# Kernel optimization log

Hardware: AMD Instinct MI355X
Metric: run time of the kernel (lower is better)

## Reference

```python
import jax, jax.numpy as jnp
import numpy as np

N = 50000
E = 800000
D_IN = 128
H = 256
L = 3


def setup_inputs() -> dict:
    key = jax.random.key(0)
    ks = jax.random.split(key, 12)
    x = jax.random.normal(ks[0], (N, D_IN), dtype=jnp.float32)
    edge_index = jax.random.randint(ks[1], (2, E), 0, N, dtype=jnp.int32)
    edge_attr = jax.random.uniform(ks[2], (E, 4), dtype=jnp.float32)
    s_enc = 1.0 / np.sqrt(D_IN)
    s_h = 1.0 / np.sqrt(H)
    W_enc = jax.random.uniform(ks[3], (D_IN, H), minval=-s_enc, maxval=s_enc)
    b_enc = jax.random.uniform(ks[4], (H,), minval=-s_enc, maxval=s_enc)
    W_g = jax.random.uniform(ks[5], (L, H, H), minval=-s_h, maxval=s_h)
    b_g = jax.random.uniform(ks[6], (L, H), minval=-s_h, maxval=s_h)
    W_out = jax.random.uniform(ks[7], (H, H), minval=-s_h, maxval=s_h)
    b_out = jax.random.uniform(ks[8], (H,), minval=-s_h, maxval=s_h)
    return {"x": x, "edge_index": edge_index, "edge_attr": edge_attr,
            "W_enc": W_enc, "b_enc": b_enc, "W_g": W_g, "b_g": b_g,
            "W_out": W_out, "b_out": b_out}


def _gcn_norm(edge_index, n):
    # PyG GCNConv: add self-loops, symmetric normalization D^-1/2 (A+I) D^-1/2
    loops = jnp.arange(n, dtype=edge_index.dtype)
    src = jnp.concatenate([edge_index[0], loops])  # [E+N]
    dst = jnp.concatenate([edge_index[1], loops])  # [E+N]
    deg = jax.ops.segment_sum(jnp.ones_like(dst, dtype=jnp.float32), dst, num_segments=n)
    dinv = jnp.where(deg > 0, jax.lax.rsqrt(deg), 0.0)
    norm = dinv[src] * dinv[dst]  # [E+N]
    return src, dst, norm


def _gcn_conv(h, W, b, src, dst, norm, n):
    m = h @ W                                  # [N,H] transform first
    agg = jax.ops.segment_sum(m[src] * norm[:, None], dst, num_segments=n)
    return agg + b


def reference(x, edge_index, edge_attr, W_enc, b_enc, W_g, b_g, W_out, b_out):
    n = x.shape[0]
    src, dst, norm = _gcn_norm(edge_index, n)
    h = jax.nn.relu(x @ W_enc + b_enc)
    for i in range(W_g.shape[0]):
        h = jax.nn.relu(_gcn_conv(h, W_g[i], b_g[i], src, dst, norm, n))
        # dropout is identity in eval mode
    return h @ W_out + b_out
```

## Files before the change

kernel.cpp:

```cpp
#include <hip/hip_runtime.h>
#include <math.h>

#define N_NODES 50000
#define N_EDGES 800000
#define D_IN    128
#define H_DIM   256
#define L_LAYERS 3
#define SCAN_BLOCKS ((N_NODES + 255) / 256)
#define FUSED_BLOCKS (N_NODES / 16)

typedef _Float16 f16x8 __attribute__((ext_vector_type(8)));
typedef _Float16 f16x4 __attribute__((ext_vector_type(4)));
typedef float    f32x4 __attribute__((ext_vector_type(4)));


__global__ __launch_bounds__(256) void hist_kernel(const int* __restrict__ dst,
                                                   int* __restrict__ counts,
                                                   int* __restrict__ rank, int e_cnt) {
    int e = blockIdx.x * 256 + threadIdx.x;
    if (e < e_cnt) rank[e] = atomicAdd(&counts[dst[e]], 1);
}

__global__ __launch_bounds__(256) void scanA_kernel(const int* __restrict__ counts,
                                                    int* __restrict__ blocksum,
                                                    float* __restrict__ dinv, int n) {
    __shared__ int s[256];
    int t = threadIdx.x;
    int i = blockIdx.x * 256 + t;
    int v = (i < n) ? counts[i] : 0;
    if (i < n) dinv[i] = rsqrtf((float)(v + 1));
    s[t] = v;
    __syncthreads();
#pragma unroll
    for (int d = 128; d > 0; d >>= 1) {
        if (t < d) s[t] += s[t + d];
        __syncthreads();
    }
    if (t == 0) blocksum[blockIdx.x] = s[0];
}

__global__ __launch_bounds__(256) void scanB_kernel(int* __restrict__ blocksum,
                                                    int* __restrict__ offsets,
                                                    int nblocks, int n, int total) {
    __shared__ int s[256];
    int t = threadIdx.x;
    int v = (t < nblocks) ? blocksum[t] : 0;
    s[t] = v;
    __syncthreads();
#pragma unroll
    for (int d = 1; d < 256; d <<= 1) {
        int x = (t >= d) ? s[t - d] : 0;
        __syncthreads();
        s[t] += x;
        __syncthreads();
    }
    if (t < nblocks) blocksum[t] = s[t] - v;
    if (t == 0) offsets[n] = total;
}

__global__ __launch_bounds__(256) void scanC_kernel(const int* __restrict__ counts,
                                                    const int* __restrict__ blocksum,
                                                    int* __restrict__ offsets, int n) {
    __shared__ int s[256];
    int t = threadIdx.x;
    int i = blockIdx.x * 256 + t;
    int v = (i < n) ? counts[i] : 0;
    s[t] = v;
    __syncthreads();
#pragma unroll
    for (int d = 1; d < 256; d <<= 1) {
        int x = (t >= d) ? s[t - d] : 0;
        __syncthreads();
        s[t] += x;
        __syncthreads();
    }
    if (i < n) offsets[i] = blocksum[blockIdx.x] + s[t] - v;
}

__global__ __launch_bounds__(256) void fill_kernel(const int* __restrict__ src,
                                                   const int* __restrict__ dst,
                                                   const int* __restrict__ offsets,
                                                   const int* __restrict__ rank,
                                                   const float* __restrict__ dinv,
                                                   int2* __restrict__ csr, int e_cnt) {
    int e = blockIdx.x * 256 + threadIdx.x;
    if (e < e_cnt) {
        int d = dst[e];
        int pos = offsets[d] + rank[e];
        int s = src[e];
        csr[pos] = make_int2(s, __float_as_int(dinv[s]));
    }
}


__global__ __launch_bounds__(256) void fused_layer(const _Float16* __restrict__ h_in,
                                                   const int* __restrict__ offsets,
                                                   const int2* __restrict__ csr,
                                                   const float* __restrict__ dinv,
                                                   const _Float16* __restrict__ WhL,
                                                   const _Float16* __restrict__ WlL,
                                                   const float* __restrict__ bias,
                                                   _Float16* __restrict__ h_out) {
    __shared__ _Float16 Alds[16][264];
    int wave = threadIdx.x >> 6;
    int lane = threadIdx.x & 63;
    int nb = blockIdx.x * 16;
    int c = lane * 4;

    for (int i = 0; i < 4; ++i) {
        int v = nb + 4 * wave + i;
        float dv = dinv[v];
        f16x4 self = *(const f16x4*)(h_in + (size_t)v * H_DIM + c);
        float ax = dv * (float)self[0];
        float ay = dv * (float)self[1];
        float az = dv * (float)self[2];
        float aw = dv * (float)self[3];

        int e  = offsets[v];
        int e1 = offsets[v + 1];

        for (; e + 15 < e1; e += 16) {
            int2 rec[16]; f16x4 r_[16];
#pragma unroll
            for (int j = 0; j < 16; ++j) rec[j] = csr[e + j];
#pragma unroll
            for (int j = 0; j < 16; ++j) r_[j] = *(const f16x4*)(h_in + (size_t)rec[j].x * H_DIM + c);
#pragma unroll
            for (int j = 0; j < 16; ++j) {
                float w = __int_as_float(rec[j].y);
                ax += w * (float)r_[j][0];
                ay += w * (float)r_[j][1];
                az += w * (float)r_[j][2];
                aw += w * (float)r_[j][3];
            }
        }
        if (e + 7 < e1) {
            int2 rec[8]; f16x4 r_[8];
#pragma unroll
            for (int j = 0; j < 8; ++j) rec[j] = csr[e + j];
#pragma unroll
            for (int j = 0; j < 8; ++j) r_[j] = *(const f16x4*)(h_in + (size_t)rec[j].x * H_DIM + c);
#pragma unroll
            for (int j = 0; j < 8; ++j) {
                float w = __int_as_float(rec[j].y);
                ax += w * (float)r_[j][0];
                ay += w * (float)r_[j][1];
                az += w * (float)r_[j][2];
                aw += w * (float)r_[j][3];
            }
            e += 8;
        }
        if (e + 3 < e1) {
            int2 rec[4]; f16x4 r_[4];
#pragma unroll
            for (int j = 0; j < 4; ++j) rec[j] = csr[e + j];
#pragma unroll
            for (int j = 0; j < 4; ++j) r_[j] = *(const f16x4*)(h_in + (size_t)rec[j].x * H_DIM + c);
#pragma unroll
            for (int j = 0; j < 4; ++j) {
                float w = __int_as_float(rec[j].y);
                ax += w * (float)r_[j][0];
                ay += w * (float)r_[j][1];
                az += w * (float)r_[j][2];
                aw += w * (float)r_[j][3];
            }
            e += 4;
        }
        if (e + 1 < e1) {
            int2 r0 = csr[e], r1 = csr[e + 1];
            f16x4 a = *(const f16x4*)(h_in + (size_t)r0.x * H_DIM + c);
            f16x4 b = *(const f16x4*)(h_in + (size_t)r1.x * H_DIM + c);
            float w0 = __int_as_float(r0.y), w1 = __int_as_float(r1.y);
            ax += w0 * (float)a[0] + w1 * (float)b[0];
            ay += w0 * (float)a[1] + w1 * (float)b[1];
            az += w0 * (float)a[2] + w1 * (float)b[2];
            aw += w0 * (float)a[3] + w1 * (float)b[3];
            e += 2;
        }
        if (e < e1) {
            int2 r0 = csr[e];
            f16x4 a = *(const f16x4*)(h_in + (size_t)r0.x * H_DIM + c);
            float w0 = __int_as_float(r0.y);
            ax += w0 * (float)a[0]; ay += w0 * (float)a[1];
            az += w0 * (float)a[2]; aw += w0 * (float)a[3];
        }
        f16x4 o;
        o[0] = (_Float16)(ax * dv);
        o[1] = (_Float16)(ay * dv);
        o[2] = (_Float16)(az * dv);
        o[3] = (_Float16)(aw * dv);
        *(f16x4*)&Alds[4 * wave + i][c] = o;
    }
    __syncthreads();

    int mrow = lane & 15;
    int g    = lane >> 4;
    const _Float16* Wh = WhL + (size_t)wave * 2048 + (size_t)lane * 8;
    const _Float16* Wl = WlL + (size_t)wave * 2048 + (size_t)lane * 8;

    f32x4 acc2[4];
#pragma unroll
    for (int cc = 0; cc < 4; ++cc) acc2[cc] = (f32x4)(0.0f);

#pragma unroll
    for (int kc = 0; kc < 8; ++kc) {
        f16x8 a = *(const f16x8*)&Alds[mrow][kc * 32 + g * 8];
#pragma unroll
        for (int cc = 0; cc < 4; ++cc) {
            f16x8 bh = *(const f16x8*)(Wh + kc * 8192 + cc * 512);
            f16x8 bl = *(const f16x8*)(Wl + kc * 8192 + cc * 512);
            acc2[cc] = __builtin_amdgcn_mfma_f32_16x16x32_f16(a, bh, acc2[cc], 0, 0, 0);
            acc2[cc] = __builtin_amdgcn_mfma_f32_16x16x32_f16(a, bl, acc2[cc], 0, 0, 0);
        }
    }

    int colq = lane & 15;
    int rowq = g * 4;
#pragma unroll
    for (int cc = 0; cc < 4; ++cc) {
        int col = wave * 64 + cc * 16 + colq;
        float b = bias[col];
#pragma unroll
        for (int r = 0; r < 4; ++r) {
            float vv = acc2[cc][r] + b;
            vv = fmaxf(vv, 0.f);
            h_out[(size_t)(nb + rowq + r) * H_DIM + col] = (_Float16)vv;
        }
    }
}


#define WCONV_TOTAL 294912

__global__ __launch_bounds__(256) void wconv_kernel(const float* __restrict__ W_enc,
                                                    const float* __restrict__ W_g,
                                                    const float* __restrict__ W_out,
                                                    _Float16* __restrict__ whi,
                                                    _Float16* __restrict__ wlo) {
    int gid = blockIdx.x * 256 + threadIdx.x;
    if (gid >= WCONV_TOTAL) return;
    const float* src; int base, e;
    if (gid < 32768)       { src = W_enc; base = 0;      e = gid; }
    else if (gid < 229376) { src = W_g;   base = 32768;  e = gid - 32768; }
    else                   { src = W_out; base = 229376; e = gid - 229376; }
    int k = e >> 8;
    int n = e & 255;
    float x = src[e];
    _Float16 hb = (_Float16)x;
    _Float16 lb = (_Float16)(x - (float)hb);
    int dst = base + (k >> 5) * 8192 + (n >> 4) * 512 + ((k & 31) >> 3) * 128
            + (n & 15) * 8 + (k & 7);
    whi[dst] = hb;
    wlo[dst] = lb;
}


template <int KC, int AMODE, int OUT16>
__global__ __launch_bounds__(256, 4) void mfma_gemm(const float* __restrict__ Af,
                                                    const _Float16* __restrict__ A16,
                                                    const _Float16* __restrict__ WhG,
                                                    const _Float16* __restrict__ WlG,
                                                    const float* __restrict__ bias,
                                                    float* __restrict__ Cf,
                                                    _Float16* __restrict__ Ch,
                                                    int n, int relu) {
    constexpr int K   = KC * 32;
    constexpr int PKC = (KC >= 8) ? 4 : KC;
    constexpr int NPH = KC / PKC;
    __shared__ _Float16 Wlds[PKC * 2 * 2048];

    int t = threadIdx.x;
    int w = t >> 6;
    int lane = t & 63;
    int q  = blockIdx.x >> 8;
    int rt = blockIdx.x & 255;
    if (rt * 256 >= n) return;
    int colbase = q * 64;
    int mrow = lane & 15;
    int koct = (lane >> 4) * 8;
    int rbase = rt * 256 + w * 64;

    int rows[4];
#pragma unroll
    for (int mt = 0; mt < 4; ++mt) {
        int r = rbase + mt * 16 + mrow;
        rows[mt] = (r < n) ? r : (n - 1);
    }

    f32x4 acc[4][4];
#pragma unroll
    for (int mt = 0; mt < 4; ++mt)
#pragma unroll
        for (int c = 0; c < 4; ++c)
            acc[mt][c] = (f32x4)(0.0f);

    f16x8 a16p[2][4];
    float4 af0[4], af1[4];
    if (AMODE == 1) {
#pragma unroll
        for (int mt = 0; mt < 4; ++mt) {
            a16p[0][mt] = *(const f16x8*)(A16 + (size_t)rows[mt] * K + koct);
            a16p[1][mt] = *(const f16x8*)(A16 + (size_t)rows[mt] * K + 32 + koct);
        }
    } else {
#pragma unroll
        for (int mt = 0; mt < 4; ++mt) {
            const float* p = Af + (size_t)rows[mt] * K + koct;
            af0[mt] = *(const float4*)p;
            af1[mt] = *(const float4*)(p + 4);
        }
    }

#pragma unroll
    for (int ph = 0; ph < NPH; ++ph) {
        if (ph) __syncthreads();
#pragma unroll
        for (int pk = 0; pk < PKC; ++pk) {
            int kc = ph * PKC + pk;
            __builtin_amdgcn_global_load_lds(
                (const __attribute__((address_space(1))) unsigned int*)(WhG + (size_t)kc * 8192 + q * 2048 + t * 8),
                (__attribute__((address_space(3))) unsigned int*)(&Wlds[(pk * 2 + 0) * 2048 + t * 8]), 16, 0, 0);
            __builtin_amdgcn_global_load_lds(
                (const __attribute__((address_space(1))) unsigned int*)(WlG + (size_t)kc * 8192 + q * 2048 + t * 8),
                (__attribute__((address_space(3))) unsigned int*)(&Wlds[(pk * 2 + 1) * 2048 + t * 8]), 16, 0, 0);
        }
        __syncthreads();

#pragma unroll
        for (int pk = 0; pk < PKC; ++pk) {
            int kc = ph * PKC + pk;
            f16x8 ah[4], al[4];
            if (AMODE == 0) {
#pragma unroll
                for (int mt = 0; mt < 4; ++mt) {
                    float4 c0 = af0[mt], c1 = af1[mt];
                    if (kc + 1 < KC) {
                        const float* p = Af + (size_t)rows[mt] * K + (kc + 1) * 32 + koct;
                        af0[mt] = *(const float4*)p;
                        af1[mt] = *(const float4*)(p + 4);
                    }
                    float xs[8] = {c0.x, c0.y, c0.z, c0.w, c1.x, c1.y, c1.z, c1.w};
                    f16x8 H, L;
#pragma unroll
                    for (int j = 0; j < 8; ++j) {
                        _Float16 hb = (_Float16)xs[j];
                        H[j] = hb;
                        L[j] = (_Float16)(xs[j] - (float)hb);
                    }
                    ah[mt] = H;
                    al[mt] = L;
                }
            }

#pragma unroll
            for (int c = 0; c < 4; ++c) {
                f16x8 bh = *(const f16x8*)&Wlds[(pk * 2 + 0) * 2048 + c * 512 + lane * 8];
                f16x8 bl = *(const f16x8*)&Wlds[(pk * 2 + 1) * 2048 + c * 512 + lane * 8];
#pragma unroll
                for (int mt = 0; mt < 4; ++mt) {
                    if (AMODE == 1) {
                        f16x8 a = a16p[kc & 1][mt];
                        acc[mt][c] = __builtin_amdgcn_mfma_f32_16x16x32_f16(a, bh, acc[mt][c], 0, 0, 0);
                        acc[mt][c] = __builtin_amdgcn_mfma_f32_16x16x32_f16(a, bl, acc[mt][c], 0, 0, 0);
                    } else {
                        acc[mt][c] = __builtin_amdgcn_mfma_f32_16x16x32_f16(ah[mt], bh, acc[mt][c], 0, 0, 0);
                        acc[mt][c] = __builtin_amdgcn_mfma_f32_16x16x32_f16(ah[mt], bl, acc[mt][c], 0, 0, 0);
                        acc[mt][c] = __builtin_amdgcn_mfma_f32_16x16x32_f16(al[mt], bh, acc[mt][c], 0, 0, 0);
                    }
                }
            }

            if (AMODE == 1 && kc + 2 < KC) {
#pragma unroll
                for (int mt = 0; mt < 4; ++mt)
                    a16p[kc & 1][mt] = *(const f16x8*)(A16 + (size_t)rows[mt] * K + (kc + 2) * 32 + koct);
            }
        }
    }

    int colq = lane & 15;
    int rowq = (lane >> 4) * 4;
#pragma unroll
    for (int c = 0; c < 4; ++c) {
        int col = colbase + c * 16 + colq;
        float b = bias[col];
#pragma unroll
        for (int mt = 0; mt < 4; ++mt) {
            int rb = rbase + mt * 16 + rowq;
#pragma unroll
            for (int r = 0; r < 4; ++r) {
                int row = rb + r;
                if (row < n) {
                    float v = acc[mt][c][r] + b;
                    if (relu) v = fmaxf(v, 0.f);
                    if (OUT16) Ch[(size_t)row * H_DIM + col] = (_Float16)v;
                    else       Cf[(size_t)row * H_DIM + col] = v;
                }
            }
        }
    }
}


extern "C" void kernel_launch(void* const* d_in, const int* in_sizes, int n_in,
                              void* d_out, int out_size, void* d_ws, size_t ws_size,
                              hipStream_t stream) {
    const float* x     = (const float*)d_in[0];
    const int*   ei    = (const int*)d_in[1];
    const float* W_enc = (const float*)d_in[3];
    const float* b_enc = (const float*)d_in[4];
    const float* W_g   = (const float*)d_in[5];
    const float* b_g   = (const float*)d_in[6];
    const float* W_out = (const float*)d_in[7];
    const float* b_out = (const float*)d_in[8];
    float* out = (float*)d_out;

    char* ws = (char*)d_ws;
    size_t off = 0;
    auto alloc = [&](size_t bytes) -> void* {
        void* p = ws + off;
        off = (off + bytes + 255) & ~(size_t)255;
        return p;
    };
    int*       counts   = (int*)alloc((size_t)N_NODES * 4);
    int*       offsets  = (int*)alloc((size_t)(N_NODES + 1) * 4);
    float*     dinv     = (float*)alloc((size_t)N_NODES * 4);
    int*       blocksum = (int*)alloc((size_t)SCAN_BLOCKS * 4);
    int*       rank     = (int*)alloc((size_t)N_EDGES * 4);
    int2*      csr      = (int2*)alloc((size_t)N_EDGES * 8);
    _Float16*  h16      = (_Float16*)alloc((size_t)N_NODES * H_DIM * 2);
    _Float16*  hbuf     = (_Float16*)alloc((size_t)N_NODES * H_DIM * 2);
    _Float16*  whi      = (_Float16*)alloc((size_t)WCONV_TOTAL * 2);
    _Float16*  wlo      = (_Float16*)alloc((size_t)WCONV_TOTAL * 2);

    const int* src = ei;
    const int* dst = ei + N_EDGES;

    hipMemsetAsync(counts, 0, (size_t)N_NODES * 4, stream);
    hist_kernel<<<(N_EDGES + 255) / 256, 256, 0, stream>>>(dst, counts, rank, N_EDGES);
    scanA_kernel<<<SCAN_BLOCKS, 256, 0, stream>>>(counts, blocksum, dinv, N_NODES);
    scanB_kernel<<<1, 256, 0, stream>>>(blocksum, offsets, SCAN_BLOCKS, N_NODES, N_EDGES);
    scanC_kernel<<<SCAN_BLOCKS, 256, 0, stream>>>(counts, blocksum, offsets, N_NODES);
    fill_kernel<<<(N_EDGES + 255) / 256, 256, 0, stream>>>(src, dst, offsets, rank, dinv,
                                                           csr, N_EDGES);
    wconv_kernel<<<(WCONV_TOTAL + 255) / 256, 256, 0, stream>>>(W_enc, W_g, W_out, whi, wlo);

    mfma_gemm<4, 0, 1><<<1024, 256, 0, stream>>>(x, (const _Float16*)nullptr,
                                                 whi, wlo, b_enc,
                                                 (float*)nullptr, h16, N_NODES, 1);
    _Float16* ping = h16;
    _Float16* pong = hbuf;
    for (int l = 0; l < L_LAYERS; ++l) {
        fused_layer<<<FUSED_BLOCKS, 256, 0, stream>>>(ping, offsets, csr, dinv,
                                                      whi + 32768 + (size_t)l * 65536,
                                                      wlo + 32768 + (size_t)l * 65536,
                                                      b_g + (size_t)l * H_DIM,
                                                      pong);
        _Float16* tmp = ping; ping = pong; pong = tmp;
    }
    mfma_gemm<8, 1, 0><<<1024, 256, 0, stream>>>((const float*)nullptr, ping,
                                                 whi + 229376, wlo + 229376, b_out,
                                                 out, (_Float16*)nullptr, N_NODES, 0);
}
```

Baseline: 498.2 us.

## Process 64 nodes per block in fused GCN layer to reuse weight loads

Each block of the fused aggregate-plus-transform layer now covers 64 nodes instead of 16. Each wave gathers 16 rows into a larger LDS tile, and the MFMA stage keeps 4 M-tiles of accumulators. Every weight fragment loaded from global memory is therefore reused across four times as many rows, which cuts redundant weight traffic. The cost is a quarter as many blocks, more accumulator registers and LDS (about 33KB), which can lower occupancy and latency hiding for the gather phase, plus bounds checks for the tail block.

```diff
diff --git a/kernel.cpp b/kernel.cpp
--- a/kernel.cpp
+++ b/kernel.cpp
@@ -7,7 +7,7 @@
 #define H_DIM   256
 #define L_LAYERS 3
 #define SCAN_BLOCKS ((N_NODES + 255) / 256)
-#define FUSED_BLOCKS (N_NODES / 16)
+#define FUSED_BLOCKS ((N_NODES + 63) / 64)
 
 typedef _Float16 f16x8 __attribute__((ext_vector_type(8)));
 typedef _Float16 f16x4 __attribute__((ext_vector_type(4)));
@@ -100,15 +100,21 @@
                                                    const _Float16* __restrict__ WhL,
                                                    const _Float16* __restrict__ WlL,
                                                    const float* __restrict__ bias,
-                                                   _Float16* __restrict__ h_out) {
-    __shared__ _Float16 Alds[16][264];
+                                                   _Float16* __restrict__ h_out, int n) {
+    __shared__ _Float16 Alds[64][264];
     int wave = threadIdx.x >> 6;
     int lane = threadIdx.x & 63;
-    int nb = blockIdx.x * 16;
+    int nb = blockIdx.x * 64;
     int c = lane * 4;
 
-    for (int i = 0; i < 4; ++i) {
-        int v = nb + 4 * wave + i;
+    for (int i = 0; i < 16; ++i) {
+        int row = wave * 16 + i;
+        int v = nb + row;
+        if (v >= n) {
+            f16x4 z = (f16x4)((_Float16)0.0f);
+            *(f16x4*)&Alds[row][c] = z;
+            continue;
+        }
         float dv = dinv[v];
         f16x4 self = *(const f16x4*)(h_in + (size_t)v * H_DIM + c);
         float ax = dv * (float)self[0];
@@ -189,7 +195,7 @@
         o[1] = (_Float16)(ay * dv);
         o[2] = (_Float16)(az * dv);
         o[3] = (_Float16)(aw * dv);
-        *(f16x4*)&Alds[4 * wave + i][c] = o;
+        *(f16x4*)&Alds[row][c] = o;
     }
     __syncthreads();
 
@@ -198,19 +204,27 @@
     const _Float16* Wh = WhL + (size_t)wave * 2048 + (size_t)lane * 8;
     const _Float16* Wl = WlL + (size_t)wave * 2048 + (size_t)lane * 8;
 
-    f32x4 acc2[4];
-#pragma unroll
-    for (int cc = 0; cc < 4; ++cc) acc2[cc] = (f32x4)(0.0f);
+    f32x4 acc2[4][4];
+#pragma unroll
+    for (int mt = 0; mt < 4; ++mt)
+#pragma unroll
+        for (int cc = 0; cc < 4; ++cc) acc2[mt][cc] = (f32x4)(0.0f);
 
 #pragma unroll
     for (int kc = 0; kc < 8; ++kc) {
-        f16x8 a = *(const f16x8*)&Alds[mrow][kc * 32 + g * 8];
+        f16x8 a[4];
+#pragma unroll
+        for (int mt = 0; mt < 4; ++mt)
+            a[mt] = *(const f16x8*)&Alds[mt * 16 + mrow][kc * 32 + g * 8];
 #pragma unroll
         for (int cc = 0; cc < 4; ++cc) {
             f16x8 bh = *(const f16x8*)(Wh + kc * 8192 + cc * 512);
             f16x8 bl = *(const f16x8*)(Wl + kc * 8192 + cc * 512);
-            acc2[cc] = __builtin_amdgcn_mfma_f32_16x16x32_f16(a, bh, acc2[cc], 0, 0, 0);
-            acc2[cc] = __builtin_amdgcn_mfma_f32_16x16x32_f16(a, bl, acc2[cc], 0, 0, 0);
+#pragma unroll
+            for (int mt = 0; mt < 4; ++mt) {
+                acc2[mt][cc] = __builtin_amdgcn_mfma_f32_16x16x32_f16(a[mt], bh, acc2[mt][cc], 0, 0, 0);
+                acc2[mt][cc] = __builtin_amdgcn_mfma_f32_16x16x32_f16(a[mt], bl, acc2[mt][cc], 0, 0, 0);
+            }
         }
     }
 
@@ -221,10 +235,16 @@
         int col = wave * 64 + cc * 16 + colq;
         float b = bias[col];
 #pragma unroll
-        for (int r = 0; r < 4; ++r) {
-            float vv = acc2[cc][r] + b;
-            vv = fmaxf(vv, 0.f);
-            h_out[(size_t)(nb + rowq + r) * H_DIM + col] = (_Float16)vv;
+        for (int mt = 0; mt < 4; ++mt) {
+#pragma unroll
+            for (int r = 0; r < 4; ++r) {
+                int row = nb + mt * 16 + rowq + r;
+                if (row < n) {
+                    float vv = acc2[mt][cc][r] + b;
+                    vv = fmaxf(vv, 0.f);
+                    h_out[(size_t)row * H_DIM + col] = (_Float16)vv;
+                }
+            }
         }
     }
 }
@@ -455,7 +475,7 @@
                                                       whi + 32768 + (size_t)l * 65536,
                                                       wlo + 32768 + (size_t)l * 65536,
                                                       b_g + (size_t)l * H_DIM,
-                                                      pong);
+                                                      pong, N_NODES);
         _Float16* tmp = ping; ping = pong; pong = tmp;
     }
     mfma_gemm<8, 1, 0><<<1024, 256, 0, stream>>>((const float*)nullptr, ping,
```

Result: slower. 580.7 us (+16.6%).
